# Performance work log

Hardware: AMD Instinct MI355X
Metric: run time of the kernel (lower is better)

Reference implementation:

```python
import jax, jax.numpy as jnp
import numpy as np

SCALE = 1.0 / np.float32(64.0 ** 0.5)  # hardcoded in source, not sqrt(d)


def setup_inputs() -> dict:
    key = jax.random.key(0)
    k1, k2 = jax.random.split(key)
    B, S, D, O = 8, 2048, 768, 768
    x = jax.random.normal(k1, (B, S, D), dtype=jnp.float32)
    kernel = jax.random.normal(k2, (3, D, O), dtype=jnp.float32) * 0.02
    return {"x": x, "kernel": kernel}


def reference(x, kernel):
    # x: [B,S,D], kernel: [3,D,O]
    WQ = jnp.einsum('bsd,do->bso', x, kernel[0])
    WK = jnp.einsum('bsd,do->bso', x, kernel[1])
    WV = jnp.einsum('bsd,do->bso', x, kernel[2])
    QK = jnp.einsum('bqo,bko->bqk', WQ, WK) * SCALE  # [B,S,S]
    A = jax.nn.softmax(QK, axis=-1)
    return jnp.einsum('bqk,bko->bqo', A, WV)  # [B,S,O]
```

## Files before the change

kernel.cpp:

```cpp
#include <hip/hip_runtime.h>

typedef unsigned short u16;
typedef __attribute__((ext_vector_type(8))) short short8;
typedef __attribute__((ext_vector_type(4))) float f32x4;
typedef __attribute__((ext_vector_type(8))) unsigned short ushort8;
typedef __attribute__((ext_vector_type(4))) unsigned short ushort4v;

__device__ __forceinline__ u16 f2bf(float f) {
    unsigned int u = __float_as_uint(f);
    u += 0x7FFFu + ((u >> 16) & 1u);
    return (u16)(u >> 16);
}
__device__ __forceinline__ float bf2f(u16 h) {
    return __uint_as_float(((unsigned int)h) << 16);
}

__device__ __forceinline__ void gld_lds16(const void* g, void* l) {
    __builtin_amdgcn_global_load_lds(
        (const __attribute__((address_space(1))) unsigned int*)g,
        (__attribute__((address_space(3))) unsigned int*)l,
        16, 0, 0);
}

template <int MODE>
__global__ __launch_bounds__(256) void gemm_bt(
    const u16* __restrict__ A, const u16* __restrict__ B,
    void* __restrict__ O0, void* __restrict__ O1, void* __restrict__ O2,
    float alpha)
{
    constexpr int K   = (MODE == 2) ? 2048 : 768;
    constexpr int lda = (MODE == 2) ? 2048 : 768;
    constexpr int ldb = (MODE == 2) ? 2048 : 768;

    __shared__ u16 As[128 * 32];
    __shared__ u16 Bs[128 * 32];

    const int f = blockIdx.x;
    const int xcd = f & 7;
    const int u = f >> 3;

    int tm, bn, cn, which = 0;
    long aoff = 0, boff = 0;
    if constexpr (MODE == 0) {
        const int c = u >> 4;
        const int rl = u & 15;
        tm = (xcd * 16 + rl) * 128;
        bn = c * 128;
        which = c / 6;
        cn = (c % 6) * 128;
    } else if constexpr (MODE == 1) {
        const int p = u >> 6, t = u & 63, c = t >> 2, rl = t & 3;
        tm = (p * 4 + rl) * 128;
        bn = cn = c * 128;
        aoff = (long)xcd * 2048 * 768;
        boff = aoff;
    } else {
        const int p = u / 12, t = u % 12, c = t >> 1, rl = t & 1;
        tm = (p * 2 + rl) * 128;
        bn = cn = c * 128;
        aoff = (long)xcd * 2048 * 2048;
        boff = (long)xcd * 768 * 2048;
    }

    const u16* Ab = A + aoff;
    const u16* Bb = B + boff;

    const int tid  = threadIdx.x;
    const int lane = tid & 63;
    const int wave = tid >> 6;
    const int wr = wave >> 1;
    const int wc = wave & 1;

    f32x4 acc[4][4] = {};

    const int swz = ((lane >> 4) ^ ((lane >> 1) & 3)) * 8;
    const u16* a_base = As + (wr * 64 + (lane & 15)) * 32 + swz;
    const u16* b_base = Bs + (wc * 64 + (lane & 15)) * 32 + swz;

    const int s0 = tid, s1 = tid + 256;
    const int r0 = s0 >> 2, kc0 = (s0 & 3) ^ ((r0 >> 1) & 3);
    const int r1 = s1 >> 2, kc1 = (s1 & 3) ^ ((r1 >> 1) & 3);
    const long ar0 = (long)(tm + r0) * lda + kc0 * 8;
    const long ar1 = (long)(tm + r1) * lda + kc1 * 8;
    const long br0 = (long)(bn + r0) * ldb + kc0 * 8;
    const long br1 = (long)(bn + r1) * ldb + kc1 * 8;

    for (int k0 = 0; k0 < K; k0 += 32) {
        __syncthreads();
        gld_lds16(Ab + ar0 + k0, (void*)(As + s0 * 8));
        gld_lds16(Ab + ar1 + k0, (void*)(As + s1 * 8));
        gld_lds16(Bb + br0 + k0, (void*)(Bs + s0 * 8));
        gld_lds16(Bb + br1 + k0, (void*)(Bs + s1 * 8));
        __syncthreads();

        short8 a[4], b[4];
#pragma unroll
        for (int i = 0; i < 4; ++i) a[i] = *(const short8*)(a_base + i * 16 * 32);
#pragma unroll
        for (int j = 0; j < 4; ++j) b[j] = *(const short8*)(b_base + j * 16 * 32);
#pragma unroll
        for (int i = 0; i < 4; ++i)
#pragma unroll
            for (int j = 0; j < 4; ++j)
                acc[i][j] = __builtin_amdgcn_mfma_f32_16x16x32_bf16(
                    a[i], b[j], acc[i][j], 0, 0, 0);
    }

#pragma unroll
    for (int i = 0; i < 4; ++i) {
        const int row0 = tm + wr * 64 + i * 16 + ((lane >> 4) << 2);
#pragma unroll
        for (int j = 0; j < 4; ++j) {
            const int col = cn + wc * 64 + j * 16 + (lane & 15);
#pragma unroll
            for (int r = 0; r < 4; ++r) {
                const int row = row0 + r;
                const float val = acc[i][j][r] * alpha;
                if constexpr (MODE == 0) {
                    if (which == 0)
                        ((u16*)O0)[(long)row * 768 + col] = f2bf(val);
                    else if (which == 1)
                        ((u16*)O1)[(long)row * 768 + col] = f2bf(val);
                    else
                        ((u16*)O2)[((long)(row >> 11) * 768 + col) * 2048 + (row & 2047)] = f2bf(val);
                } else if constexpr (MODE == 1) {
                    ((u16*)O0)[(long)xcd * 2048 * 2048 + (long)row * 2048 + col] = f2bf(val);
                } else {
                    ((float*)O0)[(long)xcd * 2048 * 768 + (long)row * 768 + col] = val;
                }
            }
        }
    }
}

__global__ __launch_bounds__(256) void cvt_x_kernel(
    const float4* __restrict__ x, ushort4v* __restrict__ out, int n4)
{
    int i = blockIdx.x * 256 + threadIdx.x;
    if (i < n4) {
        float4 f = x[i];
        ushort4v o;
        o.x = f2bf(f.x); o.y = f2bf(f.y); o.z = f2bf(f.z); o.w = f2bf(f.w);
        out[i] = o;
    }
}

__global__ __launch_bounds__(256) void cvt_w_kernel(
    const float* __restrict__ w, u16* __restrict__ wt)
{
    int i = blockIdx.x * 256 + threadIdx.x;
    int d = i % 768;
    int o = (i / 768) % 768;
    int m = i / (768 * 768);
    wt[i] = f2bf(w[((long)m * 768 + d) * 768 + o]);
}

__global__ __launch_bounds__(256) void softmax_kernel(u16* __restrict__ S)
{
    const long row = blockIdx.x;
    u16* p = S + row * 2048;
    const int t = threadIdx.x;
    const int lane = t & 63;
    const int wave = t >> 6;
    __shared__ float red[8];

    ushort8 raw = *(const ushort8*)(p + t * 8);
    float v[8];
    float m = -1e30f;
#pragma unroll
    for (int i = 0; i < 8; ++i) { v[i] = bf2f(raw[i]); m = fmaxf(m, v[i]); }
#pragma unroll
    for (int off = 1; off < 64; off <<= 1) m = fmaxf(m, __shfl_xor(m, off, 64));
    if (lane == 0) red[wave] = m;
    __syncthreads();
    m = fmaxf(fmaxf(red[0], red[1]), fmaxf(red[2], red[3]));

    float s = 0.f;
#pragma unroll
    for (int i = 0; i < 8; ++i) { v[i] = __expf(v[i] - m); s += v[i]; }
#pragma unroll
    for (int off = 1; off < 64; off <<= 1) s += __shfl_xor(s, off, 64);
    if (lane == 0) red[4 + wave] = s;
    __syncthreads();
    s = (red[4] + red[5]) + (red[6] + red[7]);

    const float inv = 1.0f / s;
    ushort8 out;
#pragma unroll
    for (int i = 0; i < 8; ++i) out[i] = f2bf(v[i] * inv);
    *(ushort8*)(p + t * 8) = out;
}

extern "C" void kernel_launch(void* const* d_in, const int* in_sizes, int n_in,
                              void* d_out, int out_size, void* d_ws, size_t ws_size,
                              hipStream_t stream)
{
    const float* x  = (const float*)d_in[0];
    const float* wk = (const float*)d_in[1];
    float* out = (float*)d_out;

    char* ws = (char*)d_ws;
    u16* xbf = (u16*)(ws);
    u16* wt  = (u16*)(ws + 25165824);
    u16* qbf = (u16*)(ws + 28704768);
    u16* kbf = (u16*)(ws + 53870592);
    u16* vt  = (u16*)(ws + 79036416);
    u16* S   = (u16*)(ws + 104202240);

    cvt_x_kernel<<<dim3(12288), dim3(256), 0, stream>>>(
        (const float4*)x, (ushort4v*)xbf, 3145728);
    cvt_w_kernel<<<dim3(6912), dim3(256), 0, stream>>>(wk, wt);

    gemm_bt<0><<<dim3(2304), dim3(256), 0, stream>>>(
        xbf, wt, qbf, kbf, vt, 1.0f);

    gemm_bt<1><<<dim3(2048), dim3(256), 0, stream>>>(
        qbf, kbf, S, nullptr, nullptr, 0.125f);

    softmax_kernel<<<dim3(16384), dim3(256), 0, stream>>>(S);

    gemm_bt<2><<<dim3(768), dim3(256), 0, stream>>>(
        S, vt, out, nullptr, nullptr, 1.0f);
}
```

Measured before the change: 355.8 us.

## Replace 128x128 GEMM with 256x256 tile, 8-wave, double-buffered pipelined kernel

Replaces the single-buffered 128x128x32 GEMM with a 256x256x64 tile kernel using 512 threads, 128 KB of LDS, and a ping-pong schedule. Global-to-LDS loads for upcoming k-tiles are interleaved with MFMA quadrants, with barriers and vmcnt waits and setprio around the MFMA bursts. The larger tile raises arithmetic intensity and the schedule hides load latency behind compute. In exchange, the grid shrinks (192 blocks for the final GEMM), so occupancy and wave balance suffer, and the hand-tuned wait counts add correctness risk.

```diff
diff --git a/kernel.cpp b/kernel.cpp
--- a/kernel.cpp
+++ b/kernel.cpp
@@ -22,18 +22,21 @@
         16, 0, 0);
 }
 
+#define WAITV(N) asm volatile("s_waitcnt vmcnt(" #N ")" ::: "memory")
+#define BAR()    __builtin_amdgcn_s_barrier()
+
 template <int MODE>
-__global__ __launch_bounds__(256) void gemm_bt(
+__global__ __launch_bounds__(512, 2) void gemm256(
     const u16* __restrict__ A, const u16* __restrict__ B,
     void* __restrict__ O0, void* __restrict__ O1, void* __restrict__ O2,
     float alpha)
 {
     constexpr int K   = (MODE == 2) ? 2048 : 768;
+    constexpr int NKT = K / 64;
     constexpr int lda = (MODE == 2) ? 2048 : 768;
     constexpr int ldb = (MODE == 2) ? 2048 : 768;
 
-    __shared__ u16 As[128 * 32];
-    __shared__ u16 Bs[128 * 32];
+    __shared__ u16 lds[65536];
 
     const int f = blockIdx.x;
     const int xcd = f & 7;
@@ -42,73 +45,107 @@
     int tm, bn, cn, which = 0;
     long aoff = 0, boff = 0;
     if constexpr (MODE == 0) {
-        const int c = u >> 4;
-        const int rl = u & 15;
-        tm = (xcd * 16 + rl) * 128;
-        bn = c * 128;
-        which = c / 6;
-        cn = (c % 6) * 128;
+        const int c = u >> 3, rl = u & 7;
+        tm = (xcd * 8 + rl) * 256;
+        bn = c * 256;
+        which = c / 3;
+        cn = (c % 3) * 256;
     } else if constexpr (MODE == 1) {
-        const int p = u >> 6, t = u & 63, c = t >> 2, rl = t & 3;
-        tm = (p * 4 + rl) * 128;
-        bn = cn = c * 128;
+        const int c = u >> 3, rl = u & 7;
+        tm = rl * 256;
+        bn = cn = c * 256;
         aoff = (long)xcd * 2048 * 768;
         boff = aoff;
     } else {
-        const int p = u / 12, t = u % 12, c = t >> 1, rl = t & 1;
-        tm = (p * 2 + rl) * 128;
-        bn = cn = c * 128;
+        const int c = u >> 3, rl = u & 7;
+        tm = rl * 256;
+        bn = cn = c * 256;
         aoff = (long)xcd * 2048 * 2048;
         boff = (long)xcd * 768 * 2048;
     }
-
-    const u16* Ab = A + aoff;
-    const u16* Bb = B + boff;
 
     const int tid  = threadIdx.x;
     const int lane = tid & 63;
     const int wave = tid >> 6;
-    const int wr = wave >> 1;
-    const int wc = wave & 1;
-
-    f32x4 acc[4][4] = {};
-
-    const int swz = ((lane >> 4) ^ ((lane >> 1) & 3)) * 8;
-    const u16* a_base = As + (wr * 64 + (lane & 15)) * 32 + swz;
-    const u16* b_base = Bs + (wc * 64 + (lane & 15)) * 32 + swz;
-
-    const int s0 = tid, s1 = tid + 256;
-    const int r0 = s0 >> 2, kc0 = (s0 & 3) ^ ((r0 >> 1) & 3);
-    const int r1 = s1 >> 2, kc1 = (s1 & 3) ^ ((r1 >> 1) & 3);
-    const long ar0 = (long)(tm + r0) * lda + kc0 * 8;
-    const long ar1 = (long)(tm + r1) * lda + kc1 * 8;
-    const long br0 = (long)(bn + r0) * ldb + kc0 * 8;
-    const long br1 = (long)(bn + r1) * ldb + kc1 * 8;
-
-    for (int k0 = 0; k0 < K; k0 += 32) {
-        __syncthreads();
-        gld_lds16(Ab + ar0 + k0, (void*)(As + s0 * 8));
-        gld_lds16(Ab + ar1 + k0, (void*)(As + s1 * 8));
-        gld_lds16(Bb + br0 + k0, (void*)(Bs + s0 * 8));
-        gld_lds16(Bb + br1 + k0, (void*)(Bs + s1 * 8));
-        __syncthreads();
-
-        short8 a[4], b[4];
-#pragma unroll
-        for (int i = 0; i < 4; ++i) a[i] = *(const short8*)(a_base + i * 16 * 32);
-#pragma unroll
-        for (int j = 0; j < 4; ++j) b[j] = *(const short8*)(b_base + j * 16 * 32);
-#pragma unroll
-        for (int i = 0; i < 4; ++i)
-#pragma unroll
-            for (int j = 0; j < 4; ++j)
-                acc[i][j] = __builtin_amdgcn_mfma_f32_16x16x32_bf16(
-                    a[i], b[j], acc[i][j], 0, 0, 0);
-    }
-
-#pragma unroll
-    for (int i = 0; i < 4; ++i) {
-        const int row0 = tm + wr * 64 + i * 16 + ((lane >> 4) << 2);
+    const int wr = wave >> 2;
+    const int wc = wave & 3;
+
+    const int srow = tid >> 3;
+    const int gcol = ((tid & 7) ^ (srow & 7)) << 3;
+    const int sdst = tid * 8;
+    const u16* Ag = A + aoff + (long)(tm + srow) * lda + gcol;
+    const u16* Bg = B + boff + (long)(bn + srow) * ldb + gcol;
+
+#define STAGE_A(KT, BO, H) do { \
+    const u16* _g = Ag + (long)(KT) * 64 + (long)(H) * 128 * lda; \
+    gld_lds16(_g,                  lds + (BO) + (H) * 8192 + sdst); \
+    gld_lds16(_g + 64 * (long)lda, lds + (BO) + (H) * 8192 + 4096 + sdst); \
+} while (0)
+#define STAGE_B(KT, BO, H) do { \
+    const u16* _g = Bg + (long)(KT) * 64 + (long)(H) * 128 * ldb; \
+    gld_lds16(_g,                  lds + 32768 + (BO) + (H) * 8192 + sdst); \
+    gld_lds16(_g + 64 * (long)ldb, lds + 32768 + (BO) + (H) * 8192 + 4096 + sdst); \
+} while (0)
+
+    const int rrow = lane & 15;
+    const int g0 = (lane >> 4) ^ (lane & 7);
+    const u16* a_rd0 = lds + (wr * 128 + rrow) * 64 + g0 * 8;
+    const u16* a_rd1 = lds + (wr * 128 + rrow) * 64 + (g0 ^ 4) * 8;
+    const u16* b_rd0 = lds + 32768 + (wc * 64 + rrow) * 64 + g0 * 8;
+    const u16* b_rd1 = lds + 32768 + (wc * 64 + rrow) * 64 + (g0 ^ 4) * 8;
+
+    short8 a[4][2], b[4][2];
+    f32x4 acc[8][4] = {};
+
+#define RD_A(BO, MH) do { _Pragma("unroll") \
+    for (int m = 0; m < 4; ++m) { \
+        a[m][0] = *(const short8*)(a_rd0 + (BO) + (MH) * 4096 + m * 1024); \
+        a[m][1] = *(const short8*)(a_rd1 + (BO) + (MH) * 4096 + m * 1024); } \
+} while (0)
+#define RD_B(BO, NH) do { _Pragma("unroll") \
+    for (int n = 0; n < 2; ++n) { \
+        b[(NH) * 2 + n][0] = *(const short8*)(b_rd0 + (BO) + ((NH) * 2 + n) * 1024); \
+        b[(NH) * 2 + n][1] = *(const short8*)(b_rd1 + (BO) + ((NH) * 2 + n) * 1024); } \
+} while (0)
+#define QUAD(MH, NH) do { \
+    __builtin_amdgcn_s_setprio(1); \
+    _Pragma("unroll") for (int ks = 0; ks < 2; ++ks) \
+    _Pragma("unroll") for (int m = 0; m < 4; ++m) \
+    _Pragma("unroll") for (int n = 0; n < 2; ++n) \
+        acc[(MH) * 4 + m][(NH) * 2 + n] = __builtin_amdgcn_mfma_f32_16x16x32_bf16( \
+            a[m][ks], b[(NH) * 2 + n][ks], acc[(MH) * 4 + m][(NH) * 2 + n], 0, 0, 0); \
+    __builtin_amdgcn_s_setprio(0); \
+} while (0)
+
+#define KTILE(KT, BO, BO_N) do { \
+    RD_A(BO, 0); RD_B(BO, 0); \
+    if ((KT) + 1 < NKT) STAGE_A((KT) + 1, BO_N, 0); \
+    BAR(); QUAD(0, 0); BAR(); \
+    RD_B(BO, 1); \
+    if ((KT) + 1 < NKT) STAGE_A((KT) + 1, BO_N, 1); \
+    BAR(); QUAD(0, 1); BAR(); \
+    RD_A(BO, 1); \
+    if ((KT) + 2 < NKT) STAGE_B((KT) + 2, BO, 0); \
+    BAR(); QUAD(1, 1); BAR(); \
+    if ((KT) + 2 < NKT) { STAGE_B((KT) + 2, BO, 1); WAITV(4); } else { WAITV(0); } \
+    BAR(); QUAD(1, 0); BAR(); \
+} while (0)
+
+    STAGE_A(0, 0, 0); STAGE_A(0, 0, 1);
+    STAGE_B(0, 0, 0); STAGE_B(0, 0, 1);
+    STAGE_B(1, 16384, 0); STAGE_B(1, 16384, 1);
+    WAITV(4);
+    BAR();
+
+#pragma unroll 1
+    for (int kt = 0; kt < NKT; kt += 2) {
+        KTILE(kt, 0, 16384);
+        KTILE(kt + 1, 16384, 0);
+    }
+
+#pragma unroll
+    for (int i = 0; i < 8; ++i) {
+        const int row0 = tm + wr * 128 + i * 16 + ((lane >> 4) << 2);
 #pragma unroll
         for (int j = 0; j < 4; ++j) {
             const int col = cn + wc * 64 + j * 16 + (lane & 15);
@@ -131,6 +168,12 @@
             }
         }
     }
+#undef KTILE
+#undef QUAD
+#undef RD_A
+#undef RD_B
+#undef STAGE_A
+#undef STAGE_B
 }
 
 __global__ __launch_bounds__(256) void cvt_x_kernel(
@@ -211,14 +254,14 @@
         (const float4*)x, (ushort4v*)xbf, 3145728);
     cvt_w_kernel<<<dim3(6912), dim3(256), 0, stream>>>(wk, wt);
 
-    gemm_bt<0><<<dim3(2304), dim3(256), 0, stream>>>(
+    gemm256<0><<<dim3(576), dim3(512), 0, stream>>>(
         xbf, wt, qbf, kbf, vt, 1.0f);
 
-    gemm_bt<1><<<dim3(2048), dim3(256), 0, stream>>>(
+    gemm256<1><<<dim3(512), dim3(512), 0, stream>>>(
         qbf, kbf, S, nullptr, nullptr, 0.125f);
 
     softmax_kernel<<<dim3(16384), dim3(256), 0, stream>>>(S);
 
-    gemm_bt<2><<<dim3(768), dim3(256), 0, stream>>>(
+    gemm256<2><<<dim3(192), dim3(512), 0, stream>>>(
         S, vt, out, nullptr, nullptr, 1.0f);
 }
```

New measurement: 348.1 us. 1.02x faster.

## Double-buffer LDS tiles in bf16 GEMM to overlap global loads with MFMA

Applied to the files above, without the earlier changes.

The shared GEMM kernel now uses two LDS buffers for the A and B tiles. It issues the async global-to-LDS loads for the next 32-wide K slice before running the MFMAs on the current slice, with one barrier per slice instead of two. This aims to hide global memory latency behind matrix-core work in all three GEMM stages. It doubles LDS use per block to 32 KB, which could lower occupancy, and it relies on the barrier waiting for the async LDS loads.

```diff
diff --git a/kernel.cpp b/kernel.cpp
--- a/kernel.cpp
+++ b/kernel.cpp
@@ -32,8 +32,8 @@
     constexpr int lda = (MODE == 2) ? 2048 : 768;
     constexpr int ldb = (MODE == 2) ? 2048 : 768;
 
-    __shared__ u16 As[128 * 32];
-    __shared__ u16 Bs[128 * 32];
+    __shared__ u16 As[2 * 128 * 32];
+    __shared__ u16 Bs[2 * 128 * 32];
 
     const int f = blockIdx.x;
     const int xcd = f & 7;
@@ -85,26 +85,42 @@
     const long br0 = (long)(bn + r0) * ldb + kc0 * 8;
     const long br1 = (long)(bn + r1) * ldb + kc1 * 8;
 
-    for (int k0 = 0; k0 < K; k0 += 32) {
+#define STAGE(BUF, K0) do { \
+    gld_lds16(Ab + ar0 + (K0), (void*)(As + (BUF) + s0 * 8)); \
+    gld_lds16(Ab + ar1 + (K0), (void*)(As + (BUF) + s1 * 8)); \
+    gld_lds16(Bb + br0 + (K0), (void*)(Bs + (BUF) + s0 * 8)); \
+    gld_lds16(Bb + br1 + (K0), (void*)(Bs + (BUF) + s1 * 8)); \
+} while (0)
+
+#define COMPUTE(BUF) do { \
+    short8 a[4], b[4]; \
+    _Pragma("unroll") \
+    for (int i = 0; i < 4; ++i) a[i] = *(const short8*)(a_base + (BUF) + i * 16 * 32); \
+    _Pragma("unroll") \
+    for (int j = 0; j < 4; ++j) b[j] = *(const short8*)(b_base + (BUF) + j * 16 * 32); \
+    _Pragma("unroll") \
+    for (int i = 0; i < 4; ++i) \
+    _Pragma("unroll") \
+        for (int j = 0; j < 4; ++j) \
+            acc[i][j] = __builtin_amdgcn_mfma_f32_16x16x32_bf16( \
+                a[i], b[j], acc[i][j], 0, 0, 0); \
+} while (0)
+
+    STAGE(0, 0);
+    __syncthreads();
+
+#pragma unroll 1
+    for (int k0 = 0; k0 < K; k0 += 64) {
+        STAGE(4096, k0 + 32);
+        COMPUTE(0);
         __syncthreads();
-        gld_lds16(Ab + ar0 + k0, (void*)(As + s0 * 8));
-        gld_lds16(Ab + ar1 + k0, (void*)(As + s1 * 8));
-        gld_lds16(Bb + br0 + k0, (void*)(Bs + s0 * 8));
-        gld_lds16(Bb + br1 + k0, (void*)(Bs + s1 * 8));
+        if (k0 + 64 < K) STAGE(0, k0 + 64);
+        COMPUTE(4096);
         __syncthreads();
-
-        short8 a[4], b[4];
-#pragma unroll
-        for (int i = 0; i < 4; ++i) a[i] = *(const short8*)(a_base + i * 16 * 32);
-#pragma unroll
-        for (int j = 0; j < 4; ++j) b[j] = *(const short8*)(b_base + j * 16 * 32);
-#pragma unroll
-        for (int i = 0; i < 4; ++i)
-#pragma unroll
-            for (int j = 0; j < 4; ++j)
-                acc[i][j] = __builtin_amdgcn_mfma_f32_16x16x32_bf16(
-                    a[i], b[j], acc[i][j], 0, 0, 0);
-    }
+    }
+
+#undef STAGE
+#undef COMPUTE
 
 #pragma unroll
     for (int i = 0; i < 4; ++i) {
```

After: 364.3 us. 2.4% more time.
